# Performance work log

Hardware: AMD Instinct MI355X
Metric: run time of the kernel (lower is better)

## Reference

```python
import jax, jax.numpy as jnp
import numpy as np

H, D, K = 8, 64, 9           # new num heads, head size, conv kernel size
A = H * D                    # all_head_size = 512
HID = 2 * A                  # input hidden size = 1024
STD = 0.02


def setup_inputs() -> dict:
    key = jax.random.key(0)
    ks = jax.random.split(key, 16)
    B, S = 4, 2048
    f = jnp.float32
    inp = {
        'hidden_states': jax.random.normal(ks[0], (B, S, HID), f),
        'Wq': jax.random.normal(ks[1], (A, A), f) * STD,
        'bq': jnp.zeros((A,), f),
        'Wk': jax.random.normal(ks[2], (A, A), f) * STD,
        'bk': jnp.zeros((A,), f),
        'Wv': jax.random.normal(ks[3], (A, A), f) * STD,
        'bv': jnp.zeros((A,), f),
        'dw_w': jax.random.normal(ks[4], (A, 1, K), f) * STD,   # depthwise conv (groups=A)
        'pw_w': jax.random.normal(ks[5], (A, A, 1), f) * STD,   # pointwise 1x1 conv
        'sep_b': jnp.zeros((A, 1), f),                          # SeparableConv1D bias
        'Wck': jax.random.normal(ks[6], (H * K, A), f) * STD,   # conv_kernel_layer
        'bck': jnp.zeros((H * K,), f),
        'Wco': jax.random.normal(ks[7], (A, A), f) * STD,       # conv_out_layer
        'bco': jnp.zeros((A,), f),
    }
    return inp


def reference(hidden_states, Wq, bq, Wk, bk, Wv, bv, dw_w, pw_w, sep_b, Wck, bck, Wco, bco):
    B, S, _ = hidden_states.shape
    hs_attn = hidden_states[:, :, :A]
    hs_conv = hidden_states[:, :, A:]

    q = hs_attn @ Wq.T + bq
    k = hs_attn @ Wk.T + bk
    v = hs_attn @ Wv.T + bv

    # SeparableConv1D on (B, A, S): depthwise then pointwise, plus bias
    x = hs_conv.transpose(0, 2, 1)
    x = jax.lax.conv_general_dilated(
        x, dw_w, window_strides=(1,), padding=[(K // 2, K // 2)],
        feature_group_count=A, dimension_numbers=('NCH', 'OIH', 'NCH'))
    x = jnp.einsum('bcs,oc->bos', x, pw_w[:, :, 0]) + sep_b
    mixed_key_conv = x.transpose(0, 2, 1)            # (B,S,A)

    # per-token softmax conv kernel
    conv_attn = mixed_key_conv * hs_conv
    ckl = (conv_attn @ Wck.T + bck).reshape(B, S, H, K)
    ckl = jax.nn.softmax(ckl, axis=-1)               # softmax over kernel taps

    # dynamic-span lightweight convolution (unfold -> batched matmul)
    col = hs_conv @ Wco.T + bco                      # (B,S,A)
    pad = jnp.pad(col, ((0, 0), (K // 2, K // 2), (0, 0)))
    windows = jnp.stack([pad[:, i:i + S] for i in range(K)], axis=-1)  # (B,S,A,K)
    windows = windows.reshape(B, S, H, D, K)
    conv_out = jnp.einsum('bshdk,bshk->bshd', windows, ckl)            # (B,S,H,D)

    # standard self-attention
    qh = q.reshape(B, S, H, D).transpose(0, 2, 1, 3)
    kh = k.reshape(B, S, H, D).transpose(0, 2, 1, 3)
    vh = v.reshape(B, S, H, D).transpose(0, 2, 1, 3)
    scale = jnp.asarray(1.0 / np.sqrt(D), q.dtype)
    scores = jnp.einsum('bhqd,bhkd->bhqk', qh, kh) * scale
    probs = jax.nn.softmax(scores, axis=-1)
    ctx = jnp.einsum('bhqk,bhkd->bqhd', probs, vh)   # (B,S,H,D)

    out = jnp.concatenate([ctx, conv_out], axis=2)   # (B,S,2H,D)
    return out.reshape(B, S, HID)
```

## Files before the change

### kernel.cpp

```cpp
#include <hip/hip_runtime.h>
#include <hip/hip_bf16.h>

#define NH   8
#define HD   64
#define KW   9
#define AD   512
#define HIDD 1024
#define BB   4
#define SS   2048
#define MTOK (BB*SS)
#define WSZ  262144

typedef __attribute__((ext_vector_type(8))) short short8;
typedef __attribute__((ext_vector_type(4))) float floatx4;
typedef __attribute__((ext_vector_type(16))) float floatx16;

__device__ __forceinline__ short f2bf(float f) {
    unsigned u = __float_as_uint(f);
    u = (u + 0x7FFFu + ((u >> 16) & 1u)) >> 16;
    return (short)u;
}
__device__ __forceinline__ float bf2f(short s) {
    return __uint_as_float(((unsigned)(unsigned short)s) << 16);
}
__device__ __forceinline__ float exp2_raw(float x) {
    return __builtin_amdgcn_exp2f(x);
}
__device__ __forceinline__ unsigned pkbf2(float a, float b) {
    unsigned d;
    asm("v_cvt_pk_bf16_f32 %0, %1, %2" : "=v"(d) : "v"(a), "v"(b));
    return d;
}
__device__ __forceinline__ void gl2lds16(const short* g, short* l) {
    __builtin_amdgcn_global_load_lds(
        (const __attribute__((address_space(1))) void*)g,
        (__attribute__((address_space(3))) void*)l, 16, 0, 0);
}

__global__ __launch_bounds__(256) void cvt_hs_kernel(
    const float* __restrict__ hs, short* __restrict__ hsb)
{
    int idx = blockIdx.x * 256 + threadIdx.x;
    const float* s = hs + (long)idx * 8;
    float4 a = *(const float4*)s, c = *(const float4*)(s + 4);
    short8 o;
    o[0]=f2bf(a.x); o[1]=f2bf(a.y); o[2]=f2bf(a.z); o[3]=f2bf(a.w);
    o[4]=f2bf(c.x); o[5]=f2bf(c.y); o[6]=f2bf(c.z); o[7]=f2bf(c.w);
    *(short8*)(hsb + (long)idx * 8) = o;
}

__global__ __launch_bounds__(256) void cvt_w_kernel(
    const float* __restrict__ pw, const float* __restrict__ Wco,
    const float* __restrict__ Wq, const float* __restrict__ Wk,
    const float* __restrict__ Wv, const float* __restrict__ Wck,
    const float* __restrict__ dw,
    short* __restrict__ dst, float* __restrict__ dwT)
{
    int idx = blockIdx.x * 256 + threadIdx.x;
    if (idx >= 172032) {
        int t = idx - 172032;
        if (t < AD * KW) {
            int c = t / KW, k = t - c * KW;
            dwT[k * AD + c] = dw[t];
        }
        return;
    }
    int e0 = idx * 8;
    short8 o;
    if (e0 < 5 * WSZ) {
        int w = e0 >> 18, off = e0 & (WSZ - 1);
        const float* src = (w == 0) ? pw : (w == 1) ? Wco : (w == 2) ? Wq
                         : (w == 3) ? Wk : Wv;
        float4 a = *(const float4*)(src + off), c = *(const float4*)(src + off + 4);
        o[0]=f2bf(a.x); o[1]=f2bf(a.y); o[2]=f2bf(a.z); o[3]=f2bf(a.w);
        o[4]=f2bf(c.x); o[5]=f2bf(c.y); o[6]=f2bf(c.z); o[7]=f2bf(c.w);
    } else {
        int off = e0 - 5 * WSZ;
        int row = off >> 9, col = off & 511;
        if (row < NH * KW) {
            const float* src = Wck + row * AD + col;
            float4 a = *(const float4*)src, c = *(const float4*)(src + 4);
            o[0]=f2bf(a.x); o[1]=f2bf(a.y); o[2]=f2bf(a.z); o[3]=f2bf(a.w);
            o[4]=f2bf(c.x); o[5]=f2bf(c.y); o[6]=f2bf(c.z); o[7]=f2bf(c.w);
        } else {
            for (int i = 0; i < 8; ++i) o[i] = 0;
        }
    }
    *(short8*)(dst + e0) = o;
}

__global__ __launch_bounds__(256) void dwconv_kernel(
    const short* __restrict__ hsb, const float* __restrict__ dwT,
    short* __restrict__ x1)
{
    int idx = blockIdx.x * 256 + threadIdx.x;
    int c8  = (idx & 63) * 8;
    int tok = idx >> 6;
    int s   = tok & (SS - 1);
    int b   = tok >> 11;
    const short* base = hsb + (long)(b * SS) * HIDD + AD + c8;
    float acc[8];
#pragma unroll
    for (int i = 0; i < 8; ++i) acc[i] = 0.f;
#pragma unroll
    for (int kk = 0; kk < KW; ++kk) {
        int ss2 = s + kk - KW / 2;
        if (ss2 >= 0 && ss2 < SS) {
            short8 hv = *(const short8*)(base + (long)ss2 * HIDD);
            float4 w0 = *(const float4*)(dwT + kk * AD + c8);
            float4 w1 = *(const float4*)(dwT + kk * AD + c8 + 4);
            acc[0] += w0.x * bf2f(hv[0]); acc[1] += w0.y * bf2f(hv[1]);
            acc[2] += w0.z * bf2f(hv[2]); acc[3] += w0.w * bf2f(hv[3]);
            acc[4] += w1.x * bf2f(hv[4]); acc[5] += w1.y * bf2f(hv[5]);
            acc[6] += w1.z * bf2f(hv[6]); acc[7] += w1.w * bf2f(hv[7]);
        }
    }
    short8 o;
#pragma unroll
    for (int i = 0; i < 8; ++i) o[i] = f2bf(acc[i]);
    *(short8*)(x1 + (long)tok * AD + c8) = o;
}

template<int FM, int FN, int MODE>
__global__ __launch_bounds__(256) void gemm_bf16_kernel(
    const short* __restrict__ X, int ldx, int xoff,
    const short* __restrict__ W,
    const float* __restrict__ b0p, const float* __restrict__ b1p,
    const float* __restrict__ b2p,
    const short* __restrict__ mulp, int mul_ld, int mul_off,
    void* __restrict__ Cout, short* __restrict__ vtout,
    int ldc, int N, int Kd, float oscale)
{
    constexpr int TM = 32 * FM, TN = 32 * FN;
    __shared__ __align__(16) short As[TM * 64];
    __shared__ __align__(16) short Bs[TN * 64];
    const int tid  = threadIdx.x;
    const int wv   = tid >> 6, lane = tid & 63;
    const int ln   = lane & 15, quad = lane >> 4;
    const int wm   = wv >> 1, wn = wv & 1;
    const int m0 = blockIdx.x * TM, n0 = blockIdx.y * TN;

    floatx4 acc[FM][FN];
#pragma unroll
    for (int i = 0; i < FM; ++i)
#pragma unroll
        for (int j = 0; j < FN; ++j) acc[i][j] = (floatx4){0.f, 0.f, 0.f, 0.f};

    const short* xbase = X + (long)m0 * ldx + xoff;
    const short* wbase = W + (long)n0 * Kd;

    for (int k0 = 0; k0 < Kd; k0 += 64) {
#pragma unroll
        for (int g = tid; g < TM * 8; g += 256) {
            int m = g >> 3, p = g & 7, gk = p ^ (m & 7);
            gl2lds16(xbase + (long)m * ldx + k0 + gk * 8, &As[g * 8]);
        }
#pragma unroll
        for (int g = tid; g < TN * 8; g += 256) {
            int m = g >> 3, p = g & 7, gk = p ^ (m & 7);
            gl2lds16(wbase + (long)m * Kd + k0 + gk * 8, &Bs[g * 8]);
        }
        __syncthreads();
#pragma unroll
        for (int half = 0; half < 2; ++half) {
            short8 afr[FM], bfr[FN];
#pragma unroll
            for (int i = 0; i < FM; ++i) {
                int p = (half * 4 + quad) ^ (ln & 7);
                afr[i] = *(const short8*)&As[(wm * 16 * FM + i * 16 + ln) * 64 + p * 8];
            }
#pragma unroll
            for (int j = 0; j < FN; ++j) {
                int p = (half * 4 + quad) ^ (ln & 7);
                bfr[j] = *(const short8*)&Bs[(wn * 16 * FN + j * 16 + ln) * 64 + p * 8];
            }
#pragma unroll
            for (int i = 0; i < FM; ++i)
#pragma unroll
                for (int j = 0; j < FN; ++j)
                    acc[i][j] = __builtin_amdgcn_mfma_f32_16x16x32_bf16(
                        afr[i], bfr[j], acc[i][j], 0, 0, 0);
        }
        __syncthreads();
    }

#pragma unroll
    for (int j = 0; j < FN; ++j) {
        int n = n0 + wn * 16 * FN + j * 16 + ln;
        if constexpr (MODE == 3) {
            if (n >= 1024) {
                int hh = (n - 1024) >> 6, dd = (n - 1024) & 63;
                float bv = b2p[n - 1024];
                int mblk = m0 + wm * 16 * FM;
                int bidx = mblk >> 11, sblk = mblk & (SS - 1);
                short* dst = vtout + ((long)((bidx * NH + hh) * HD + dd)) * SS + sblk;
#pragma unroll
                for (int i = 0; i < FM; ++i) {
                    unsigned lo = pkbf2(acc[i][j][0] + bv, acc[i][j][1] + bv);
                    unsigned hi = pkbf2(acc[i][j][2] + bv, acc[i][j][3] + bv);
                    *(uint2*)(dst + i * 16 + quad * 4) = make_uint2(lo, hi);
                }
            } else {
                float bv = (n < 512) ? b0p[n] : b1p[n - 512];
                float sc = (n < 512) ? oscale : 1.f;
#pragma unroll
                for (int i = 0; i < FM; ++i) {
#pragma unroll
                    for (int r = 0; r < 4; ++r) {
                        int m = m0 + wm * 16 * FM + i * 16 + quad * 4 + r;
                        float val = (acc[i][j][r] + bv) * sc;
                        ((short*)Cout)[(long)m * ldc + n] = f2bf(val);
                    }
                }
            }
        } else if (n < N) {
            float bv = b0p[n], sc = oscale;
#pragma unroll
            for (int i = 0; i < FM; ++i) {
#pragma unroll
                for (int r = 0; r < 4; ++r) {
                    int m = m0 + wm * 16 * FM + i * 16 + quad * 4 + r;
                    float val = (acc[i][j][r] + bv) * sc;
                    if constexpr (MODE == 2)
                        val *= bf2f(mulp[(long)m * mul_ld + mul_off + n]);
                    if constexpr (MODE == 0)
                        ((float*)Cout)[(long)m * ldc + n] = val;
                    else
                        ((short*)Cout)[(long)m * ldc + n] = f2bf(val);
                }
            }
        }
    }
}

__global__ __launch_bounds__(256) void convout_kernel(
    const short* __restrict__ col, const float* __restrict__ ckl,
    float* __restrict__ out)
{
    int idx = blockIdx.x * 256 + threadIdx.x;
    int d4  = (idx & 127) * 4;
    int tok = idx >> 7;
    int s   = tok & (SS - 1);
    int b   = tok >> 11;
    int h   = d4 >> 6;
    const float* lg = ckl + (long)tok * (NH * KW) + h * KW;
    float wv[KW];
    float mx = -1e30f;
#pragma unroll
    for (int i = 0; i < KW; ++i) { wv[i] = lg[i]; mx = fmaxf(mx, wv[i]); }
    float sum = 0.f;
#pragma unroll
    for (int i = 0; i < KW; ++i) { wv[i] = __expf(wv[i] - mx); sum += wv[i]; }
    float inv = 1.f / sum;
    float a0 = 0.f, a1 = 0.f, a2 = 0.f, a3 = 0.f;
    const short* cbase = col + (long)(b * SS) * AD + d4;
#pragma unroll
    for (int kk = 0; kk < KW; ++kk) {
        int ss2 = s + kk - KW / 2;
        if (ss2 >= 0 && ss2 < SS) {
            uint2 cv = *(const uint2*)(cbase + (long)ss2 * AD);
            float w = wv[kk];
            a0 += w * bf2f((short)(cv.x & 0xFFFF));
            a1 += w * bf2f((short)(cv.x >> 16));
            a2 += w * bf2f((short)(cv.y & 0xFFFF));
            a3 += w * bf2f((short)(cv.y >> 16));
        }
    }
    *(float4*)&out[(long)tok * HIDD + AD + d4] =
        make_float4(a0 * inv, a1 * inv, a2 * inv, a3 * inv);
}

__global__ __launch_bounds__(256) void flash_mfma_kernel(
    const short* __restrict__ qkv, const short* __restrict__ vT,
    float* __restrict__ out)
{
    const int qt = blockIdx.x, h = blockIdx.y, b = blockIdx.z;
    const int tid  = threadIdx.x;
    const int w    = tid >> 6;
    const int lane = tid & 63;
    const int l5   = lane & 31;
    const int hh   = lane >> 5;

    __shared__ __align__(16) short Kb[2][64 * 64];
    __shared__ __align__(16) short Vb[2][64 * 64];
    __shared__ float ls[4][32];

    const int  q0 = qt * 128 + w * 32;
    const long rowbase = (long)b * SS;

    short8 qf[4];
    {
        const short* qrow = qkv + (rowbase + q0 + l5) * 1536 + h * HD;
#pragma unroll
        for (int i = 0; i < 4; ++i)
            qf[i] = *(const short8*)(qrow + i * 16 + hh * 8);
    }

    floatx16 acc0, acc1;
    floatx16 Z;
#pragma unroll
    for (int r = 0; r < 16; ++r) { acc0[r] = 0.f; acc1[r] = 0.f; Z[r] = 0.f; }
    float l_i = 0.f;

    const int m1 = tid >> 3,  gk1 = (tid & 7) ^ (m1 & 7);
    const int g2 = 256 + tid;
    const int m2 = g2 >> 3,   gk2 = (g2 & 7) ^ (m2 & 7);
    const short* kbase  = qkv + 512 + rowbase * 1536 + h * HD;
    const short* vtbase = vT + ((long)(b * NH + h) * HD) * SS;
    const short* sk0 = kbase  + (long)m1 * 1536 + gk1 * 8;
    const short* sk1 = kbase  + (long)m2 * 1536 + gk2 * 8;
    const short* sv0 = vtbase + (long)m1 * SS   + gk1 * 8;
    const short* sv1 = vtbase + (long)m2 * SS   + gk2 * 8;

    auto STAGE_K = [&](int buf) {
        gl2lds16(sk0, &Kb[buf][tid * 8]);
        gl2lds16(sk1, &Kb[buf][g2 * 8]);
        sk0 += 64 * 1536; sk1 += 64 * 1536;
    };
    auto STAGE_V = [&](int buf) {
        gl2lds16(sv0, &Vb[buf][tid * 8]);
        gl2lds16(sv1, &Vb[buf][g2 * 8]);
        sv0 += 64; sv1 += 64;
    };

    auto qkt = [&](const short* KB, floatx16& S0, floatx16& S1) {
        {
            int p = hh ^ (l5 & 7);
            short8 k0 = *(const short8*)&KB[l5 * 64 + p * 8];
            short8 k1 = *(const short8*)&KB[(32 + l5) * 64 + p * 8];
            S0 = __builtin_amdgcn_mfma_f32_32x32x16_bf16(k0, qf[0], Z, 0, 0, 0);
            S1 = __builtin_amdgcn_mfma_f32_32x32x16_bf16(k1, qf[0], Z, 0, 0, 0);
        }
#pragma unroll
        for (int i = 1; i < 4; ++i) {
            int p = (2 * i + hh) ^ (l5 & 7);
            short8 k0 = *(const short8*)&KB[l5 * 64 + p * 8];
            short8 k1 = *(const short8*)&KB[(32 + l5) * 64 + p * 8];
            S0 = __builtin_amdgcn_mfma_f32_32x32x16_bf16(k0, qf[i], S0, 0, 0, 0);
            S1 = __builtin_amdgcn_mfma_f32_32x32x16_bf16(k1, qf[i], S1, 0, 0, 0);
        }
    };

    auto smax = [&](const floatx16& S0, const floatx16& S1, short8* pf) {
        float pe0[16], pe1[16];
#pragma unroll
        for (int r = 0; r < 16; ++r) {
            pe0[r] = exp2_raw(S0[r]);
            pe1[r] = exp2_raw(S1[r]);
        }
        float s = 0.f;
#pragma unroll
        for (int r = 0; r < 16; ++r) s += pe0[r] + pe1[r];
        l_i += s;
#pragma unroll
        for (int t = 0; t < 2; ++t) {
            const float* pe = t ? pe1 : pe0;
#pragma unroll
            for (int u = 0; u < 2; ++u) {
                unsigned a0 = pkbf2(pe[8 * u + 0], pe[8 * u + 1]);
                unsigned a1 = pkbf2(pe[8 * u + 2], pe[8 * u + 3]);
                unsigned b0 = pkbf2(pe[8 * u + 4], pe[8 * u + 5]);
                unsigned b1 = pkbf2(pe[8 * u + 6], pe[8 * u + 7]);
                asm("v_permlane32_swap_b32 %0, %1" : "+v"(a0), "+v"(b0));
                asm("v_permlane32_swap_b32 %0, %1" : "+v"(a1), "+v"(b1));
                union { uint4 u4; short8 s8; } cv;
                cv.u4 = make_uint4(a0, a1, b0, b1);
                pf[t * 2 + u] = cv.s8;
            }
        }
    };

    auto pv = [&](const short* VB, const short8* pf) {
#pragma unroll
        for (int s = 0; s < 4; ++s) {
            int p = (2 * s + hh) ^ (l5 & 7);
            short8 v0 = *(const short8*)&VB[l5 * 64 + p * 8];
            short8 v1 = *(const short8*)&VB[(32 + l5) * 64 + p * 8];
            acc0 = __builtin_amdgcn_mfma_f32_32x32x16_bf16(pf[s], v0, acc0, 0, 0, 0);
            acc1 = __builtin_amdgcn_mfma_f32_32x32x16_bf16(pf[s], v1, acc1, 0, 0, 0);
        }
    };

    const int NT = SS / 64;
    short8 pfA[4], pfB[4];

    STAGE_K(0);
    asm volatile("s_waitcnt vmcnt(0)" ::: "memory");
    __builtin_amdgcn_s_barrier();
    asm volatile("" ::: "memory");

    {
        STAGE_K(1); STAGE_V(0);
        floatx16 S0, S1;
        qkt(Kb[0], S0, S1);
        smax(S0, S1, pfA);
        asm volatile("s_waitcnt vmcnt(0)" ::: "memory");
        __builtin_amdgcn_s_barrier();
        asm volatile("" ::: "memory");
    }

    for (int t = 1; t + 1 < NT; t += 2) {
        {
            STAGE_K(0); STAGE_V(1);
            floatx16 S0, S1;
            __builtin_amdgcn_s_setprio(1);
            qkt(Kb[1], S0, S1);
            pv(Vb[0], pfA);
            __builtin_amdgcn_s_setprio(0);
            smax(S0, S1, pfB);
            asm volatile("s_waitcnt vmcnt(0)" ::: "memory");
            __builtin_amdgcn_s_barrier();
            asm volatile("" ::: "memory");
        }
        {
            if (t + 2 < NT) STAGE_K(1);
            STAGE_V(0);
            floatx16 S0, S1;
            __builtin_amdgcn_s_setprio(1);
            qkt(Kb[0], S0, S1);
            pv(Vb[1], pfB);
            __builtin_amdgcn_s_setprio(0);
            smax(S0, S1, pfA);
            asm volatile("s_waitcnt vmcnt(0)" ::: "memory");
            __builtin_amdgcn_s_barrier();
            asm volatile("" ::: "memory");
        }
    }

    {
        STAGE_V(1);
        floatx16 S0, S1;
        __builtin_amdgcn_s_setprio(1);
        qkt(Kb[1], S0, S1);
        pv(Vb[0], pfA);
        __builtin_amdgcn_s_setprio(0);
        smax(S0, S1, pfB);
        asm volatile("s_waitcnt vmcnt(0)" ::: "memory");
        __builtin_amdgcn_s_barrier();
        asm volatile("" ::: "memory");
    }
    pv(Vb[1], pfB);

    l_i += __shfl_xor(l_i, 32);
    ls[w][l5] = 1.f / l_i;
    float4 lv[4];
#pragma unroll
    for (int g = 0; g < 4; ++g)
        lv[g] = *(const float4*)&ls[w][8 * g + 4 * hh];

#pragma unroll
    for (int r = 0; r < 16; ++r) {
        int g = r >> 2, j = r & 3;
        int qr = j + 8 * g + 4 * hh;
        float iv = lv[g][j];
        float* orow = out + (rowbase + q0 + qr) * HIDD + h * HD;
        orow[l5]      = acc0[r] * iv;
        orow[32 + l5] = acc1[r] * iv;
    }
}

extern "C" void kernel_launch(void* const* d_in, const int* in_sizes, int n_in,
                              void* d_out, int out_size, void* d_ws, size_t ws_size,
                              hipStream_t stream)
{
    const float* hs   = (const float*)d_in[0];
    const float* Wq   = (const float*)d_in[1];
    const float* bq   = (const float*)d_in[2];
    const float* Wk   = (const float*)d_in[3];
    const float* bk   = (const float*)d_in[4];
    const float* Wv   = (const float*)d_in[5];
    const float* bv   = (const float*)d_in[6];
    const float* dw   = (const float*)d_in[7];
    const float* pw   = (const float*)d_in[8];
    const float* sepb = (const float*)d_in[9];
    const float* Wck  = (const float*)d_in[10];
    const float* bck  = (const float*)d_in[11];
    const float* Wco  = (const float*)d_in[12];
    const float* bco  = (const float*)d_in[13];
    float* out = (float*)d_out;

    short* hsb  = (short*)d_ws;
    short* x1c  = hsb + (long)MTOK * HIDD;
    short* qkvb = x1c + (long)MTOK * AD;
    short* vTb  = qkvb + (long)MTOK * 1536;
    float* ckl  = (float*)(vTb + (long)MTOK * AD);
    short* wb   = (short*)(ckl + (long)MTOK * (NH * KW));
    short* pw_b   = wb;
    short* Wco_b  = wb + 1L * WSZ;
    short* Wqkv_b = wb + 2L * WSZ;
    short* Wck_b  = wb + 5L * WSZ;
    float* dwT    = (float*)(Wck_b + 128L * AD);
    short* cab    = qkvb;

    const float QSCALE = 0.18033688011112042f;

    cvt_hs_kernel<<<MTOK * HIDD / 2048, 256, 0, stream>>>(hs, hsb);
    cvt_w_kernel<<<690, 256, 0, stream>>>(
        pw, Wco, Wq, Wk, Wv, Wck, dw, wb, dwT);
    dwconv_kernel<<<MTOK * AD / 2048, 256, 0, stream>>>(hsb, dwT, x1c);
    gemm_bf16_kernel<2, 2, 2><<<dim3(MTOK / 64, AD / 64), 256, 0, stream>>>(
        x1c, AD, 0, pw_b, sepb, nullptr, nullptr, hsb, HIDD, AD,
        cab, nullptr, AD, AD, AD, 1.f);
    gemm_bf16_kernel<2, 2, 0><<<dim3(MTOK / 64, 2), 256, 0, stream>>>(
        cab, AD, 0, Wck_b, bck, nullptr, nullptr, nullptr, 0, 0,
        ckl, nullptr, NH * KW, NH * KW, AD, 1.f);
    gemm_bf16_kernel<2, 2, 1><<<dim3(MTOK / 64, AD / 64), 256, 0, stream>>>(
        hsb, HIDD, AD, Wco_b, bco, nullptr, nullptr, nullptr, 0, 0,
        x1c, nullptr, AD, AD, AD, 1.f);
    convout_kernel<<<MTOK * AD / 1024, 256, 0, stream>>>(x1c, ckl, out);
    gemm_bf16_kernel<4, 4, 3><<<dim3(MTOK / 128, 1536 / 128), 256, 0, stream>>>(
        hsb, HIDD, 0, Wqkv_b, bq, bk, bv, nullptr, 0, 0,
        qkvb, vTb, 1536, 1536, AD, QSCALE);
    flash_mfma_kernel<<<dim3(SS / 128, NH, BB), 256, 0, stream>>>(qkvb, vTb, out);

    (void)in_sizes; (void)n_in; (void)out_size; (void)ws_size;
}
```

Baseline: 229.9 us.

## Triple-buffer K/V tiles in flash attention with partial vmcnt waits

```diff
diff --git a/kernel.cpp b/kernel.cpp
--- a/kernel.cpp
+++ b/kernel.cpp
@@ -281,8 +281,8 @@
     const int l5   = lane & 31;
     const int hh   = lane >> 5;
 
-    __shared__ __align__(16) short Kb[2][64 * 64];
-    __shared__ __align__(16) short Vb[2][64 * 64];
+    __shared__ __align__(16) short Kb[3][4096];
+    __shared__ __align__(16) short Vb[3][4096];
     __shared__ float ls[4][32];
 
     const int  q0 = qt * 128 + w * 32;
@@ -312,14 +312,14 @@
     const short* sv0 = vtbase + (long)m1 * SS   + gk1 * 8;
     const short* sv1 = vtbase + (long)m2 * SS   + gk2 * 8;
 
-    auto STAGE_K = [&](int buf) {
-        gl2lds16(sk0, &Kb[buf][tid * 8]);
-        gl2lds16(sk1, &Kb[buf][g2 * 8]);
-        sk0 += 64 * 1536; sk1 += 64 * 1536;
+    auto STAGE_K = [&](int slot, bool adv) {
+        gl2lds16(sk0, &Kb[slot][tid * 8]);
+        gl2lds16(sk1, &Kb[slot][g2 * 8]);
+        if (adv) { sk0 += 64 * 1536; sk1 += 64 * 1536; }
     };
-    auto STAGE_V = [&](int buf) {
-        gl2lds16(sv0, &Vb[buf][tid * 8]);
-        gl2lds16(sv1, &Vb[buf][g2 * 8]);
+    auto STAGE_V = [&](int slot) {
+        gl2lds16(sv0, &Vb[slot][tid * 8]);
+        gl2lds16(sv1, &Vb[slot][g2 * 8]);
         sv0 += 64; sv1 += 64;
     };
 
@@ -381,54 +381,53 @@
         }
     };
 
-    const int NT = SS / 64;
     short8 pfA[4], pfB[4];
 
-    STAGE_K(0);
+    STAGE_K(0, true);
+    STAGE_K(1, true);
+    STAGE_V(0);
     asm volatile("s_waitcnt vmcnt(0)" ::: "memory");
     __builtin_amdgcn_s_barrier();
     asm volatile("" ::: "memory");
 
     {
-        STAGE_K(1); STAGE_V(0);
+        STAGE_K(2, true);
+        STAGE_V(1);
         floatx16 S0, S1;
         qkt(Kb[0], S0, S1);
         smax(S0, S1, pfA);
-        asm volatile("s_waitcnt vmcnt(0)" ::: "memory");
+        asm volatile("s_waitcnt vmcnt(4)" ::: "memory");
         __builtin_amdgcn_s_barrier();
         asm volatile("" ::: "memory");
     }
 
-    for (int t = 1; t + 1 < NT; t += 2) {
-        {
-            STAGE_K(0); STAGE_V(1);
-            floatx16 S0, S1;
-            __builtin_amdgcn_s_setprio(1);
-            qkt(Kb[1], S0, S1);
-            pv(Vb[0], pfA);
-            __builtin_amdgcn_s_setprio(0);
-            smax(S0, S1, pfB);
-            asm volatile("s_waitcnt vmcnt(0)" ::: "memory");
-            __builtin_amdgcn_s_barrier();
-            asm volatile("" ::: "memory");
-        }
-        {
-            if (t + 2 < NT) STAGE_K(1);
-            STAGE_V(0);
-            floatx16 S0, S1;
-            __builtin_amdgcn_s_setprio(1);
-            qkt(Kb[0], S0, S1);
-            pv(Vb[1], pfB);
-            __builtin_amdgcn_s_setprio(0);
-            smax(S0, S1, pfA);
-            asm volatile("s_waitcnt vmcnt(0)" ::: "memory");
-            __builtin_amdgcn_s_barrier();
-            asm volatile("" ::: "memory");
-        }
-    }
+#define PHASE(KS, VPS, KST, VST, KADV, PIN, POUT)                      \
+    {                                                                  \
+        STAGE_K(KST, KADV);                                            \
+        STAGE_V(VST);                                                  \
+        floatx16 S0, S1;                                               \
+        __builtin_amdgcn_s_setprio(1);                                 \
+        qkt(Kb[KS], S0, S1);                                           \
+        pv(Vb[VPS], PIN);                                              \
+        __builtin_amdgcn_s_setprio(0);                                 \
+        smax(S0, S1, POUT);                                            \
+        asm volatile("s_waitcnt vmcnt(4)" ::: "memory");               \
+        __builtin_amdgcn_s_barrier();                                  \
+        asm volatile("" ::: "memory");                                 \
+    }
+
+    for (int g = 0; g < 5; ++g) {
+        bool notlast = (g < 4);
+        PHASE(1, 0, 0, 2, true,    pfA, pfB);
+        PHASE(2, 1, 1, 0, true,    pfB, pfA);
+        PHASE(0, 2, 2, 1, true,    pfA, pfB);
+        PHASE(1, 0, 0, 2, true,    pfB, pfA);
+        PHASE(2, 1, 1, 0, notlast, pfA, pfB);
+        PHASE(0, 2, 2, 1, notlast, pfB, pfA);
+    }
+#undef PHASE
 
     {
-        STAGE_V(1);
         floatx16 S0, S1;
         __builtin_amdgcn_s_setprio(1);
         qkt(Kb[1], S0, S1);
```

Measured after the change: 220.1 us. 4.2% less time.
